# Kernel optimization log

Measured on AMD Instinct MI355X. Metric: run time of the kernel, lower is better.

Reference implementation:

```python
import jax, jax.numpy as jnp
import numpy as np

D = 1024        # n_embed
POS = 512       # n_pos_embed
H = 16          # heads
HS = D // H     # head size
DFF = 4 * D     # mlp hidden
EPS = 1e-5


def layernorm(x, g, b, eps=EPS):
    mu = jnp.mean(x, axis=-1, keepdims=True)
    var = jnp.var(x, axis=-1, keepdims=True)
    return (x - mu) * jax.lax.rsqrt(var + eps) * g + b


def setup_inputs() -> dict:
    key = jax.random.key(0)
    ks = jax.random.split(key, 12)
    std = 0.02
    inp = {
        "grid": jax.random.normal(ks[0], (8, 24, 24, D), dtype=jnp.float32),
        "query_pos": jax.random.normal(ks[1], (8, 1024, POS), dtype=jnp.float32),
        "Wq": jax.random.normal(ks[2], (POS, D), dtype=jnp.float32) * std,
        "Wk": jax.random.normal(ks[3], (D, D), dtype=jnp.float32) * std,
        "Wv": jax.random.normal(ks[4], (D, D), dtype=jnp.float32) * std,
        "Wo": jax.random.normal(ks[5], (D, D), dtype=jnp.float32) * std,
        "ln_grid_g": jnp.ones((D,), jnp.float32),
        "ln_grid_b": jnp.zeros((D,), jnp.float32),
        "ln_q_g": jnp.ones((POS,), jnp.float32),
        "ln_q_b": jnp.zeros((POS,), jnp.float32),
        "ln_mlp_g": jnp.ones((D,), jnp.float32),
        "ln_mlp_b": jnp.zeros((D,), jnp.float32),
        "W1": jax.random.normal(ks[6], (D, DFF), dtype=jnp.float32) * std,
        "b1": jnp.zeros((DFF,), jnp.float32),
        "W2": jax.random.normal(ks[7], (DFF, D), dtype=jnp.float32) * std,
        "b2": jnp.zeros((D,), jnp.float32),
    }
    return inp


def reference(grid, query_pos, Wq, Wk, Wv, Wo, ln_grid_g, ln_grid_b,
              ln_q_g, ln_q_b, ln_mlp_g, ln_mlp_b, W1, b1, W2, b2):
    B, N, M, d = grid.shape
    T = N * M
    grid_flat = grid.reshape(B, T, d)
    grid_norm = layernorm(grid_flat, ln_grid_g, ln_grid_b)
    K = jnp.einsum('btd,de->bte', grid_norm, Wk)
    V = jnp.einsum('btd,de->bte', grid_norm, Wv)
    query_norm = layernorm(query_pos, ln_q_g, ln_q_b)
    Q = jnp.einsum('blp,pe->ble', query_norm, Wq)
    L = Q.shape[1]
    # split heads: (B, H, L, HS)
    Qh = Q.reshape(B, L, H, HS).transpose(0, 2, 1, 3)
    Kh = K.reshape(B, T, H, HS).transpose(0, 2, 1, 3)
    Vh = V.reshape(B, T, H, HS).transpose(0, 2, 1, 3)
    scale = 1.0 / np.sqrt(HS).astype(np.float32)
    scores = jnp.einsum('bhld,bhmd->bhlm', Qh, Kh) * scale
    probs = jax.nn.softmax(scores, axis=-1)
    attn = jnp.einsum('bhlm,bhmd->bhld', probs, Vh)
    attn = attn.transpose(0, 2, 1, 3).reshape(B, L, d)
    attn = jnp.einsum('bld,de->ble', attn, Wo)
    x = Q + attn  # Q_proj residual
    x_norm = layernorm(x, ln_mlp_g, ln_mlp_b)
    mlp = jax.nn.gelu(x_norm @ W1 + b1) @ W2 + b2
    return x + mlp
```

## Files before the change

### kernel.cpp

```cpp
#include <hip/hip_runtime.h>

typedef __bf16 bf16x8 __attribute__((ext_vector_type(8)));
typedef float  f32x4  __attribute__((ext_vector_type(4)));
typedef short  s16x8  __attribute__((ext_vector_type(8)));

__device__ __forceinline__ unsigned short f2b(float f) {
  unsigned int u = __float_as_uint(f);
  u += 0x7fffu + ((u >> 16) & 1u);
  return (unsigned short)(u >> 16);
}
__device__ __forceinline__ float b2f(unsigned short h) {
  return __uint_as_float(((unsigned int)h) << 16);
}

__device__ __forceinline__ void gload_lds16(const unsigned short* g, unsigned short* l) {
  __builtin_amdgcn_global_load_lds((const __attribute__((address_space(1))) void*)g,
                                   (__attribute__((address_space(3))) void*)l, 16, 0, 0);
}

__device__ __forceinline__ void bar() {
  __builtin_amdgcn_sched_barrier(0);
  asm volatile("" ::: "memory");
  __builtin_amdgcn_s_barrier();
  asm volatile("" ::: "memory");
  __builtin_amdgcn_sched_barrier(0);
}

#define WAIT_LGKM0 do { asm volatile("s_waitcnt lgkmcnt(0)" ::: "memory"); \
                        __builtin_amdgcn_sched_barrier(0); } while (0)

__global__ __launch_bounds__(256) void transpose_w(const float* __restrict__ in,
                                                   unsigned short* __restrict__ out,
                                                   int R, int C) {
  __shared__ float t[32][33];
  int c0 = blockIdx.x * 32, r0 = blockIdx.y * 32;
  int tx = threadIdx.x & 31, ty = threadIdx.x >> 5;
  for (int i = ty; i < 32; i += 8)
    t[i][tx] = in[(size_t)(r0 + i) * C + (c0 + tx)];
  __syncthreads();
  for (int i = ty; i < 32; i += 8)
    out[(size_t)(c0 + i) * R + (r0 + tx)] = f2b(t[tx][i]);
}

__global__ __launch_bounds__(256) void transpose_v(const unsigned short* __restrict__ V,
                                                   unsigned short* __restrict__ Vt,
                                                   int vstride) {
  __shared__ unsigned short tile[64][72];
  const int t0 = blockIdx.x * 64;
  const int d0 = blockIdx.y * 64;
  const int b  = blockIdx.z;
  const int tid = threadIdx.x;
  const int r = tid >> 3, c8 = tid & 7;
#pragma unroll
  for (int p = 0; p < 2; ++p) {
    int row = p * 32 + r;
    s16x8 v = *(const s16x8*)(V + ((size_t)(b * 576 + t0 + row) * vstride + d0 + c8 * 8));
    *(s16x8*)&tile[row][c8 * 8] = v;
  }
  __syncthreads();
#pragma unroll
  for (int p = 0; p < 2; ++p) {
    int drow = p * 32 + r;
    unsigned short tmp[8];
#pragma unroll
    for (int j = 0; j < 8; ++j) tmp[j] = tile[c8 * 8 + j][drow];
    *(s16x8*)(Vt + ((size_t)(b * 1024 + d0 + drow) * 576 + t0 + c8 * 8)) = *(const s16x8*)tmp;
  }
}

__global__ __launch_bounds__(256) void ln_kernel(const float* __restrict__ in,
                                                 const float* __restrict__ g,
                                                 const float* __restrict__ b,
                                                 unsigned short* __restrict__ out,
                                                 int cols) {
  int row = blockIdx.x;
  const float* x = in + (size_t)row * cols;
  float s = 0.f, s2 = 0.f;
  for (int c = threadIdx.x * 4; c < cols; c += 1024) {
    float4 v = *(const float4*)(x + c);
    s  += v.x + v.y + v.z + v.w;
    s2 += v.x * v.x + v.y * v.y + v.z * v.z + v.w * v.w;
  }
#pragma unroll
  for (int o = 32; o > 0; o >>= 1) { s += __shfl_down(s, o); s2 += __shfl_down(s2, o); }
  __shared__ float rs[4], rs2[4];
  int w = threadIdx.x >> 6;
  if ((threadIdx.x & 63) == 0) { rs[w] = s; rs2[w] = s2; }
  __syncthreads();
  s  = rs[0] + rs[1] + rs[2] + rs[3];
  s2 = rs2[0] + rs2[1] + rs2[2] + rs2[3];
  float inv  = 1.f / (float)cols;
  float mean = s * inv;
  float var  = s2 * inv - mean * mean;
  float rstd = rsqrtf(var + 1e-5f);
  unsigned short* outp = out + (size_t)row * cols;
  for (int c = threadIdx.x * 4; c < cols; c += 1024) {
    float4 v = *(const float4*)(x + c);
    ushort4 ov;
    ov.x = f2b((v.x - mean) * rstd * g[c + 0] + b[c + 0]);
    ov.y = f2b((v.y - mean) * rstd * g[c + 1] + b[c + 1]);
    ov.z = f2b((v.z - mean) * rstd * g[c + 2] + b[c + 2]);
    ov.w = f2b((v.w - mean) * rstd * g[c + 3] + b[c + 3]);
    *(ushort4*)(outp + c) = ov;
  }
}

template <int BM, int BIAS, int GELU, int RES, int OUTBF>
__global__ __launch_bounds__(512) void gemm256(const unsigned short* __restrict__ A,
                                               const unsigned short* __restrict__ Bt,
                                               float* __restrict__ Cf,
                                               unsigned short* __restrict__ Cb,
                                               const float* __restrict__ bias,
                                               const float* __restrict__ resf,
                                               const unsigned short* __restrict__ resb,
                                               int M, int N, int K) {
  constexpr int MF = BM / 32;
  constexpr int MH = MF / 2;
  constexpr int LA = BM / 128;
  __shared__ unsigned short L[2][(BM + 256) * 64];
  const int tid = threadIdx.x;
  const int w = tid >> 6, l = tid & 63;
  const int rl = l & 15, kb = l >> 4;
  const int wm = w >> 2, wn = w & 3;
  const int m0 = blockIdx.x * BM, n0 = blockIdx.y * 256;
  const int NT = K >> 6;
  const int colsw = ((l & 7) ^ (l >> 3)) * 8;
  const int lrow = l >> 3;

  auto stage = [&](int t, int half) {
    if (t >= NT) return;
    unsigned short* base = L[t & 1];
    if (half < 2) {
      const unsigned short* g = Bt + (size_t)(n0 + half * 128) * K + t * 64;
#pragma unroll
      for (int j = 0; j < 2; ++j) {
        int row = w * 16 + j * 8;
        gload_lds16(g + (size_t)(row + lrow) * K + colsw,
                    base + BM * 64 + half * 8192 + row * 64);
      }
    } else {
      const int h = half - 2;
      const unsigned short* g = A + (size_t)(m0 + h * (BM / 2)) * K + t * 64;
#pragma unroll
      for (int j = 0; j < LA; ++j) {
        int row = w * (8 * LA) + j * 8;
        gload_lds16(g + (size_t)(row + lrow) * K + colsw,
                    base + h * (BM / 2) * 64 + row * 64);
      }
    }
  };

  f32x4 acc[MF][4];
  f32x4 zz = {0.f, 0.f, 0.f, 0.f};
#pragma unroll
  for (int i = 0; i < MF; ++i)
#pragma unroll
    for (int j = 0; j < 4; ++j) acc[i][j] = zz;

  stage(0, 0); stage(0, 1); stage(0, 2); stage(0, 3);
  stage(1, 0); stage(1, 1); stage(1, 2);

  const int aoff = wm * (BM / 2) * 64;
  const int boff = BM * 64 + (wn >> 1) * 8192 + (wn & 1) * 64 * 64;

  for (int t = 0; t < NT; ++t) {
    const unsigned short* Lb = L[t & 1];
    if (t + 1 < NT) {
      if constexpr (LA == 2) asm volatile("s_waitcnt vmcnt(6)" ::: "memory");
      else                   asm volatile("s_waitcnt vmcnt(5)" ::: "memory");
    } else {
      asm volatile("s_waitcnt vmcnt(0)" ::: "memory");
    }
    __builtin_amdgcn_sched_barrier(0);
    bar();

    bf16x8 af[MH][2], bf[4][2];
#pragma unroll
    for (int mf = 0; mf < MH; ++mf)
#pragma unroll
      for (int kf = 0; kf < 2; ++kf)
        af[mf][kf] = *(const bf16x8*)(Lb + aoff + (mf * 16 + rl) * 64 +
                                      (((kf * 4 + kb) ^ (rl & 7)) * 8));
#pragma unroll
    for (int nf = 0; nf < 4; ++nf)
#pragma unroll
      for (int kf = 0; kf < 2; ++kf)
        bf[nf][kf] = *(const bf16x8*)(Lb + boff + (nf * 16 + rl) * 64 +
                                      (((kf * 4 + kb) ^ (rl & 7)) * 8));
    stage(t + 1, 3);
    WAIT_LGKM0;
    __builtin_amdgcn_s_setprio(1);
#pragma unroll
    for (int mf = 0; mf < MH; ++mf)
#pragma unroll
      for (int nf = 0; nf < 2; ++nf)
#pragma unroll
        for (int kf = 0; kf < 2; ++kf)
          acc[mf][nf] = __builtin_amdgcn_mfma_f32_16x16x32_bf16(af[mf][kf], bf[nf][kf], acc[mf][nf], 0, 0, 0);
    __builtin_amdgcn_s_setprio(0);
    bar();

    stage(t + 2, 0);
    __builtin_amdgcn_s_setprio(1);
#pragma unroll
    for (int mf = 0; mf < MH; ++mf)
#pragma unroll
      for (int nf = 2; nf < 4; ++nf)
#pragma unroll
        for (int kf = 0; kf < 2; ++kf)
          acc[mf][nf] = __builtin_amdgcn_mfma_f32_16x16x32_bf16(af[mf][kf], bf[nf][kf], acc[mf][nf], 0, 0, 0);
    __builtin_amdgcn_s_setprio(0);
    bar();

#pragma unroll
    for (int mf = 0; mf < MH; ++mf)
#pragma unroll
      for (int kf = 0; kf < 2; ++kf)
        af[mf][kf] = *(const bf16x8*)(Lb + aoff + ((MH + mf) * 16 + rl) * 64 +
                                      (((kf * 4 + kb) ^ (rl & 7)) * 8));
    stage(t + 2, 1);
    WAIT_LGKM0;
    __builtin_amdgcn_s_setprio(1);
#pragma unroll
    for (int mf = 0; mf < MH; ++mf)
#pragma unroll
      for (int nf = 0; nf < 2; ++nf)
#pragma unroll
        for (int kf = 0; kf < 2; ++kf)
          acc[MH + mf][nf] = __builtin_amdgcn_mfma_f32_16x16x32_bf16(af[mf][kf], bf[nf][kf], acc[MH + mf][nf], 0, 0, 0);
    __builtin_amdgcn_s_setprio(0);
    bar();

    stage(t + 2, 2);
    __builtin_amdgcn_s_setprio(1);
#pragma unroll
    for (int mf = 0; mf < MH; ++mf)
#pragma unroll
      for (int nf = 2; nf < 4; ++nf)
#pragma unroll
        for (int kf = 0; kf < 2; ++kf)
          acc[MH + mf][nf] = __builtin_amdgcn_mfma_f32_16x16x32_bf16(af[mf][kf], bf[nf][kf], acc[MH + mf][nf], 0, 0, 0);
    __builtin_amdgcn_s_setprio(0);
  }

  bar();

  float bias_v[4];
  if (BIAS) {
#pragma unroll
    for (int nf = 0; nf < 4; ++nf) bias_v[nf] = bias[n0 + wn * 64 + nf * 16 + rl];
  }
  unsigned short* patch  = ((unsigned short*)L) + w * (16 * 72);
  float*          patchf = ((float*)L) + w * (16 * 72);

#pragma unroll
  for (int mf = 0; mf < MF; ++mf) {
#pragma unroll
    for (int nf = 0; nf < 4; ++nf) {
#pragma unroll
      for (int r = 0; r < 4; ++r) {
        float v = acc[mf][nf][r];
        if (BIAS) v += bias_v[nf];
        if (GELU) {
          float t2 = 1.5957691f * (v + 0.044715f * v * v * v);
          float e = __expf(fminf(t2, 60.f));
          v = v * e / (e + 1.f);
        }
        int prow = kb * 4 + r, pcol = nf * 16 + rl;
        if (OUTBF) patch[prow * 72 + pcol] = f2b(v);
        else       patchf[prow * 72 + pcol] = v;
      }
    }
    WAIT_LGKM0;
    if (OUTBF) {
#pragma unroll
      for (int half = 0; half < 2; ++half) {
        int prow = half * 8 + (l >> 3);
        int pcol = (l & 7) * 8;
        s16x8 vv = *(const s16x8*)(patch + prow * 72 + pcol);
        int grow = m0 + wm * (BM / 2) + mf * 16 + prow;
        int gcol = n0 + wn * 64 + pcol;
        *(s16x8*)(Cb + (size_t)grow * N + gcol) = vv;
      }
    } else {
#pragma unroll
      for (int p = 0; p < 4; ++p) {
        int prow = p * 4 + (l >> 4);
        int pcol = (l & 15) * 4;
        float4 vv = *(const float4*)(patchf + prow * 72 + pcol);
        int grow = m0 + wm * (BM / 2) + mf * 16 + prow;
        int gcol = n0 + wn * 64 + pcol;
        if (RES == 1) {
          float4 rv = *(const float4*)(resf + (size_t)grow * N + gcol);
          vv.x += rv.x; vv.y += rv.y; vv.z += rv.z; vv.w += rv.w;
        }
        if (RES == 2) {
          ushort4 rv = *(const ushort4*)(resb + (size_t)grow * N + gcol);
          vv.x += b2f(rv.x); vv.y += b2f(rv.y); vv.z += b2f(rv.z); vv.w += b2f(rv.w);
        }
        *(float4*)(Cf + (size_t)grow * N + gcol) = vv;
      }
    }
    WAIT_LGKM0;
  }
}

__global__ __launch_bounds__(256) void attn_mfma(const unsigned short* __restrict__ Qb,
                                                 const unsigned short* __restrict__ Kb,
                                                 const unsigned short* __restrict__ Vtb,
                                                 unsigned short* __restrict__ Ob,
                                                 int kstride) {
  __shared__ unsigned short Qs[64 * 64];
  __shared__ unsigned short Ks[2][64 * 64];
  __shared__ unsigned short Vs[2][64 * 64];
  __shared__ unsigned short Ps[64 * 64];

  const int t = threadIdx.x, w = t >> 6, l = t & 63;
  const int b = blockIdx.z, h = blockIdx.y, q0 = blockIdx.x * 64;
  const int rl = l & 15, kb = l >> 4;

  auto stage64 = [&](unsigned short* lds, const unsigned short* g, int gstride) {
#pragma unroll
    for (int p = 0; p < 2; ++p) {
      int row = p * 32 + w * 8 + (l >> 3);
      const unsigned short* src = g + (size_t)row * gstride + (((l & 7) ^ (row & 7)) * 8);
      gload_lds16(src, lds + p * 2048 + w * 512);
    }
  };

  const unsigned short* Qg = Qb + ((size_t)(b * 1024 + q0) * 1024 + h * 64);
  auto Kg = [&](int kt) { return Kb + ((size_t)(b * 576 + kt * 64) * kstride + h * 64); };
  auto Vg = [&](int kt) { return Vtb + ((size_t)(b * 1024 + h * 64) * 576 + kt * 64); };

  stage64(Qs, Qg, 1024);
  stage64(Ks[0], Kg(0), kstride);
  stage64(Vs[0], Vg(0), 576);
  __syncthreads();

  bf16x8 qf[2];
  {
    int row = w * 16 + rl;
#pragma unroll
    for (int kf = 0; kf < 2; ++kf)
      qf[kf] = *(const bf16x8*)(Qs + row * 64 + (((kf * 4 + kb) ^ (row & 7)) * 8));
  }

  float m_run[4], l_run[4];
  f32x4 accO[4];
#pragma unroll
  for (int r = 0; r < 4; ++r) { m_run[r] = -1e30f; l_run[r] = 0.f; }
  f32x4 zz = {0.f, 0.f, 0.f, 0.f};
#pragma unroll
  for (int nf = 0; nf < 4; ++nf) accO[nf] = zz;

  for (int kt = 0; kt < 9; ++kt) {
    const int buf = kt & 1;
    if (kt + 1 < 9) {
      stage64(Ks[buf ^ 1], Kg(kt + 1), kstride);
      stage64(Vs[buf ^ 1], Vg(kt + 1), 576);
    }

    f32x4 accS[4];
#pragma unroll
    for (int nf = 0; nf < 4; ++nf) accS[nf] = zz;
#pragma unroll
    for (int nf = 0; nf < 4; ++nf) {
      int row = nf * 16 + rl;
#pragma unroll
      for (int kf = 0; kf < 2; ++kf) {
        bf16x8 kfrag = *(const bf16x8*)(Ks[buf] + row * 64 + (((kf * 4 + kb) ^ (row & 7)) * 8));
        accS[nf] = __builtin_amdgcn_mfma_f32_16x16x32_bf16(qf[kf], kfrag, accS[nf], 0, 0, 0);
      }
    }

    float sv[4][4];
#pragma unroll
    for (int nf = 0; nf < 4; ++nf)
#pragma unroll
      for (int r = 0; r < 4; ++r) sv[nf][r] = accS[nf][r] * 0.125f;

    float al[4];
#pragma unroll
    for (int r = 0; r < 4; ++r) {
      float mr = fmaxf(fmaxf(sv[0][r], sv[1][r]), fmaxf(sv[2][r], sv[3][r]));
#pragma unroll
      for (int xm = 1; xm < 16; xm <<= 1) mr = fmaxf(mr, __shfl_xor(mr, xm));
      float mn = fmaxf(m_run[r], mr);
      al[r] = __expf(m_run[r] - mn);
      m_run[r] = mn;
      float rs = 0.f;
#pragma unroll
      for (int nf = 0; nf < 4; ++nf) {
        sv[nf][r] = __expf(sv[nf][r] - mn);
        rs += sv[nf][r];
      }
#pragma unroll
      for (int xm = 1; xm < 16; xm <<= 1) rs += __shfl_xor(rs, xm);
      l_run[r] = l_run[r] * al[r] + rs;
    }

#pragma unroll
    for (int nf = 0; nf < 4; ++nf)
#pragma unroll
      for (int r = 0; r < 4; ++r) {
        int q = w * 16 + kb * 4 + r;
        int col = nf * 16 + rl;
        Ps[q * 64 + (col ^ ((q & 7) << 3))] = f2b(sv[nf][r]);
      }

#pragma unroll
    for (int nf = 0; nf < 4; ++nf)
#pragma unroll
      for (int r = 0; r < 4; ++r) accO[nf][r] *= al[r];

    asm volatile("s_waitcnt lgkmcnt(0)" ::: "memory");
    __builtin_amdgcn_sched_barrier(0);

    bf16x8 pf[2];
    {
      int row = w * 16 + rl;
#pragma unroll
      for (int kf = 0; kf < 2; ++kf)
        pf[kf] = *(const bf16x8*)(Ps + row * 64 + (((kf * 4 + kb) ^ (row & 7)) * 8));
    }
#pragma unroll
    for (int nf = 0; nf < 4; ++nf) {
      int row = nf * 16 + rl;
#pragma unroll
      for (int kf = 0; kf < 2; ++kf) {
        bf16x8 vfrag = *(const bf16x8*)(Vs[buf] + row * 64 + (((kf * 4 + kb) ^ (row & 7)) * 8));
        accO[nf] = __builtin_amdgcn_mfma_f32_16x16x32_bf16(pf[kf], vfrag, accO[nf], 0, 0, 0);
      }
    }

    __syncthreads();
  }

#pragma unroll
  for (int nf = 0; nf < 4; ++nf) {
#pragma unroll
    for (int r = 0; r < 4; ++r) {
      float o = accO[nf][r] / l_run[r];
      size_t qg = (size_t)(b * 1024 + q0 + w * 16 + kb * 4 + r);
      Ob[qg * 1024 + h * 64 + nf * 16 + rl] = f2b(o);
    }
  }
}

extern "C" void kernel_launch(void* const* d_in, const int* in_sizes, int n_in,
                              void* d_out, int out_size, void* d_ws, size_t ws_size,
                              hipStream_t stream) {
  const float* grid_in = (const float*)d_in[0];
  const float* qpos    = (const float*)d_in[1];
  const float* Wq      = (const float*)d_in[2];
  const float* Wk      = (const float*)d_in[3];
  const float* Wv      = (const float*)d_in[4];
  const float* Wo      = (const float*)d_in[5];
  const float* g_grid  = (const float*)d_in[6];
  const float* b_grid  = (const float*)d_in[7];
  const float* g_q     = (const float*)d_in[8];
  const float* b_q     = (const float*)d_in[9];
  const float* g_mlp   = (const float*)d_in[10];
  const float* b_mlp   = (const float*)d_in[11];
  const float* W1      = (const float*)d_in[12];
  const float* b1      = (const float*)d_in[13];
  const float* W2      = (const float*)d_in[14];
  const float* b2      = (const float*)d_in[15];

  char* ws = (char*)d_ws;
  size_t off = 0;
  auto alloc = [&](size_t bytes) -> void* {
    void* p = ws + off;
    off = (off + bytes + 255) & ~(size_t)255;
    return p;
  };

  unsigned short* Wqt  = (unsigned short*)alloc((size_t)1024 * 512 * 2);
  unsigned short* Wkvt = (unsigned short*)alloc((size_t)2048 * 1024 * 2);
  unsigned short* Wot  = (unsigned short*)alloc((size_t)1024 * 1024 * 2);
  unsigned short* W1t  = (unsigned short*)alloc((size_t)4096 * 1024 * 2);
  unsigned short* W2t  = (unsigned short*)alloc((size_t)1024 * 4096 * 2);
  unsigned short* gn   = (unsigned short*)alloc((size_t)4608 * 1024 * 2);
  unsigned short* qn   = (unsigned short*)alloc((size_t)8192 * 512 * 2);
  unsigned short* KVb  = (unsigned short*)alloc((size_t)4608 * 2048 * 2);
  unsigned short* Qbf  = (unsigned short*)alloc((size_t)8192 * 1024 * 2);
  unsigned short* atb  = (unsigned short*)alloc((size_t)8192 * 1024 * 2);
  float*          xf   = (float*)alloc((size_t)8192 * 1024 * 4);
  unsigned short* xnb  = (unsigned short*)alloc((size_t)8192 * 1024 * 2);
  unsigned short* hb   = (unsigned short*)alloc((size_t)8192 * 4096 * 2);
  unsigned short* Vtb  = hb;
  (void)ws_size; (void)in_sizes; (void)n_in; (void)out_size;

  transpose_w<<<dim3(32, 16), 256, 0, stream>>>(Wq, Wqt, 512, 1024);
  transpose_w<<<dim3(32, 32), 256, 0, stream>>>(Wk, Wkvt, 1024, 1024);
  transpose_w<<<dim3(32, 32), 256, 0, stream>>>(Wv, Wkvt + (size_t)1024 * 1024, 1024, 1024);
  transpose_w<<<dim3(32, 32), 256, 0, stream>>>(Wo, Wot, 1024, 1024);
  transpose_w<<<dim3(128, 32), 256, 0, stream>>>(W1, W1t, 1024, 4096);
  transpose_w<<<dim3(32, 128), 256, 0, stream>>>(W2, W2t, 4096, 1024);

  ln_kernel<<<4608, 256, 0, stream>>>(grid_in, g_grid, b_grid, gn, 1024);
  ln_kernel<<<8192, 256, 0, stream>>>(qpos, g_q, b_q, qn, 512);

  gemm256<128, 0, 0, 0, 1><<<dim3(36, 8), 512, 0, stream>>>(gn, Wkvt, nullptr, KVb, nullptr, nullptr, nullptr, 4608, 2048, 1024);
  gemm256<128, 0, 0, 0, 1><<<dim3(64, 4), 512, 0, stream>>>(qn, Wqt, nullptr, Qbf, nullptr, nullptr, nullptr, 8192, 1024, 512);

  transpose_v<<<dim3(9, 16, 8), 256, 0, stream>>>(KVb + 1024, Vtb, 2048);

  attn_mfma<<<dim3(16, 16, 8), 256, 0, stream>>>(Qbf, KVb, Vtb, atb, 2048);

  gemm256<128, 0, 0, 2, 0><<<dim3(64, 4), 512, 0, stream>>>(atb, Wot, xf, nullptr, nullptr, nullptr, Qbf, 8192, 1024, 1024);

  ln_kernel<<<8192, 256, 0, stream>>>(xf, g_mlp, b_mlp, xnb, 1024);
  gemm256<256, 1, 1, 0, 1><<<dim3(32, 16), 512, 0, stream>>>(xnb, W1t, nullptr, hb, b1, nullptr, nullptr, 8192, 4096, 1024);
  gemm256<128, 1, 0, 1, 0><<<dim3(64, 4), 512, 0, stream>>>(hb, W2t, (float*)d_out, nullptr, b2, xf, nullptr, 8192, 1024, 4096);
}
```

Baseline: 368.6 us.

## Fuse K/V/Q projections into one launch, compute V transposed, transpose attention tiles

Merges the K, V and Q projection GEMMs into a single kernel that dispatches by block index. V is produced already transposed by swapping operands (Wv times grid_norm), so the separate transpose_v kernel is removed. Attention now computes S^T and O^T, which gives per-lane softmax rows with only two cross-lane shuffles and per-warp P tiles, and writes output as 4-wide vectors. This removes a kernel launch and an extra pass over V, and improves load balance, at the cost of a larger heterogeneous kernel and changed indexing.

```diff
diff --git a/kernel.cpp b/kernel.cpp
--- a/kernel.cpp
+++ b/kernel.cpp
@@ -40,32 +40,6 @@
   __syncthreads();
   for (int i = ty; i < 32; i += 8)
     out[(size_t)(c0 + i) * R + (r0 + tx)] = f2b(t[tx][i]);
-}
-
-__global__ __launch_bounds__(256) void transpose_v(const unsigned short* __restrict__ V,
-                                                   unsigned short* __restrict__ Vt,
-                                                   int vstride) {
-  __shared__ unsigned short tile[64][72];
-  const int t0 = blockIdx.x * 64;
-  const int d0 = blockIdx.y * 64;
-  const int b  = blockIdx.z;
-  const int tid = threadIdx.x;
-  const int r = tid >> 3, c8 = tid & 7;
-#pragma unroll
-  for (int p = 0; p < 2; ++p) {
-    int row = p * 32 + r;
-    s16x8 v = *(const s16x8*)(V + ((size_t)(b * 576 + t0 + row) * vstride + d0 + c8 * 8));
-    *(s16x8*)&tile[row][c8 * 8] = v;
-  }
-  __syncthreads();
-#pragma unroll
-  for (int p = 0; p < 2; ++p) {
-    int drow = p * 32 + r;
-    unsigned short tmp[8];
-#pragma unroll
-    for (int j = 0; j < 8; ++j) tmp[j] = tile[c8 * 8 + j][drow];
-    *(s16x8*)(Vt + ((size_t)(b * 1024 + d0 + drow) * 576 + t0 + c8 * 8)) = *(const s16x8*)tmp;
-  }
 }
 
 __global__ __launch_bounds__(256) void ln_kernel(const float* __restrict__ in,
@@ -106,30 +80,30 @@
 }
 
 template <int BM, int BIAS, int GELU, int RES, int OUTBF>
-__global__ __launch_bounds__(512) void gemm256(const unsigned short* __restrict__ A,
-                                               const unsigned short* __restrict__ Bt,
-                                               float* __restrict__ Cf,
-                                               unsigned short* __restrict__ Cb,
-                                               const float* __restrict__ bias,
-                                               const float* __restrict__ resf,
-                                               const unsigned short* __restrict__ resb,
-                                               int M, int N, int K) {
+__device__ __forceinline__ void gemm_body(const unsigned short* __restrict__ A,
+                                          const unsigned short* __restrict__ Bt,
+                                          float* __restrict__ Cf,
+                                          unsigned short* __restrict__ Cb,
+                                          const float* __restrict__ bias,
+                                          const float* __restrict__ resf,
+                                          const unsigned short* __restrict__ resb,
+                                          int N, int K, int m0, int n0,
+                                          unsigned short* L) {
   constexpr int MF = BM / 32;
   constexpr int MH = MF / 2;
   constexpr int LA = BM / 128;
-  __shared__ unsigned short L[2][(BM + 256) * 64];
+  constexpr int LSTEP = (BM + 256) * 64;
   const int tid = threadIdx.x;
   const int w = tid >> 6, l = tid & 63;
   const int rl = l & 15, kb = l >> 4;
   const int wm = w >> 2, wn = w & 3;
-  const int m0 = blockIdx.x * BM, n0 = blockIdx.y * 256;
   const int NT = K >> 6;
   const int colsw = ((l & 7) ^ (l >> 3)) * 8;
   const int lrow = l >> 3;
 
   auto stage = [&](int t, int half) {
     if (t >= NT) return;
-    unsigned short* base = L[t & 1];
+    unsigned short* base = L + (t & 1) * LSTEP;
     if (half < 2) {
       const unsigned short* g = Bt + (size_t)(n0 + half * 128) * K + t * 64;
 #pragma unroll
@@ -164,7 +138,7 @@
   const int boff = BM * 64 + (wn >> 1) * 8192 + (wn & 1) * 64 * 64;
 
   for (int t = 0; t < NT; ++t) {
-    const unsigned short* Lb = L[t & 1];
+    const unsigned short* Lb = L + (t & 1) * LSTEP;
     if (t + 1 < NT) {
       if constexpr (LA == 2) asm volatile("s_waitcnt vmcnt(6)" ::: "memory");
       else                   asm volatile("s_waitcnt vmcnt(5)" ::: "memory");
@@ -250,7 +224,7 @@
 #pragma unroll
     for (int nf = 0; nf < 4; ++nf) bias_v[nf] = bias[n0 + wn * 64 + nf * 16 + rl];
   }
-  unsigned short* patch  = ((unsigned short*)L) + w * (16 * 72);
+  unsigned short* patch  = L + w * (16 * 72);
   float*          patchf = ((float*)L) + w * (16 * 72);
 
 #pragma unroll
@@ -305,15 +279,52 @@
   }
 }
 
+template <int BM, int BIAS, int GELU, int RES, int OUTBF>
+__global__ __launch_bounds__(512) void gemm256(const unsigned short* __restrict__ A,
+                                               const unsigned short* __restrict__ Bt,
+                                               float* __restrict__ Cf,
+                                               unsigned short* __restrict__ Cb,
+                                               const float* __restrict__ bias,
+                                               const float* __restrict__ resf,
+                                               const unsigned short* __restrict__ resb,
+                                               int N, int K) {
+  __shared__ unsigned short L[2 * (BM + 256) * 64];
+  gemm_body<BM, BIAS, GELU, RES, OUTBF>(A, Bt, Cf, Cb, bias, resf, resb, N, K,
+                                        blockIdx.x * BM, blockIdx.y * 256, L);
+}
+
+__global__ __launch_bounds__(512) void kvq_gemm(const unsigned short* __restrict__ gn,
+                                                const unsigned short* __restrict__ Wkt,
+                                                unsigned short* __restrict__ Kb,
+                                                const unsigned short* __restrict__ Wvt,
+                                                unsigned short* __restrict__ Vt2,
+                                                const unsigned short* __restrict__ qn,
+                                                const unsigned short* __restrict__ Wqt,
+                                                unsigned short* __restrict__ Qbf) {
+  __shared__ unsigned short L[2 * (128 + 256) * 64];
+  const int x = blockIdx.x;
+  if (x < 144) {
+    gemm_body<128, 0, 0, 0, 1>(gn, Wkt, nullptr, Kb, nullptr, nullptr, nullptr,
+                               1024, 1024, (x % 36) * 128, (x / 36) * 256, L);
+  } else if (x < 288) {
+    const int x2 = x - 144;
+    gemm_body<128, 0, 0, 0, 1>(Wvt, gn, nullptr, Vt2, nullptr, nullptr, nullptr,
+                               4608, 1024, (x2 % 8) * 128, (x2 / 8) * 256, L);
+  } else {
+    const int x3 = x - 288;
+    gemm_body<128, 0, 0, 0, 1>(qn, Wqt, nullptr, Qbf, nullptr, nullptr, nullptr,
+                               1024, 512, (x3 % 64) * 128, (x3 / 64) * 256, L);
+  }
+}
+
 __global__ __launch_bounds__(256) void attn_mfma(const unsigned short* __restrict__ Qb,
                                                  const unsigned short* __restrict__ Kb,
                                                  const unsigned short* __restrict__ Vtb,
-                                                 unsigned short* __restrict__ Ob,
-                                                 int kstride) {
+                                                 unsigned short* __restrict__ Ob) {
   __shared__ unsigned short Qs[64 * 64];
   __shared__ unsigned short Ks[2][64 * 64];
   __shared__ unsigned short Vs[2][64 * 64];
-  __shared__ unsigned short Ps[64 * 64];
+  __shared__ unsigned short PsT[4][16 * 64];
 
   const int t = threadIdx.x, w = t >> 6, l = t & 63;
   const int b = blockIdx.z, h = blockIdx.y, q0 = blockIdx.x * 64;
@@ -329,12 +340,12 @@
   };
 
   const unsigned short* Qg = Qb + ((size_t)(b * 1024 + q0) * 1024 + h * 64);
-  auto Kg = [&](int kt) { return Kb + ((size_t)(b * 576 + kt * 64) * kstride + h * 64); };
-  auto Vg = [&](int kt) { return Vtb + ((size_t)(b * 1024 + h * 64) * 576 + kt * 64); };
+  auto Kg = [&](int kt) { return Kb + ((size_t)(b * 576 + kt * 64) * 1024 + h * 64); };
+  auto Vg = [&](int kt) { return Vtb + ((size_t)(h * 64) * 4608 + b * 576 + kt * 64); };
 
   stage64(Qs, Qg, 1024);
-  stage64(Ks[0], Kg(0), kstride);
-  stage64(Vs[0], Vg(0), 576);
+  stage64(Ks[0], Kg(0), 1024);
+  stage64(Vs[0], Vg(0), 4608);
   __syncthreads();
 
   bf16x8 qf[2];
@@ -345,19 +356,19 @@
       qf[kf] = *(const bf16x8*)(Qs + row * 64 + (((kf * 4 + kb) ^ (row & 7)) * 8));
   }
 
-  float m_run[4], l_run[4];
-  f32x4 accO[4];
-#pragma unroll
-  for (int r = 0; r < 4; ++r) { m_run[r] = -1e30f; l_run[r] = 0.f; }
+  float m_run = -1e30f, l_run = 0.f;
+  f32x4 accOT[4];
   f32x4 zz = {0.f, 0.f, 0.f, 0.f};
 #pragma unroll
-  for (int nf = 0; nf < 4; ++nf) accO[nf] = zz;
+  for (int df = 0; df < 4; ++df) accOT[df] = zz;
+
+  unsigned short* pw = &PsT[w][0];
 
   for (int kt = 0; kt < 9; ++kt) {
     const int buf = kt & 1;
     if (kt + 1 < 9) {
-      stage64(Ks[buf ^ 1], Kg(kt + 1), kstride);
-      stage64(Vs[buf ^ 1], Vg(kt + 1), 576);
+      stage64(Ks[buf ^ 1], Kg(kt + 1), 1024);
+      stage64(Vs[buf ^ 1], Vg(kt + 1), 4608);
     }
 
     f32x4 accS[4];
@@ -369,7 +380,7 @@
 #pragma unroll
       for (int kf = 0; kf < 2; ++kf) {
         bf16x8 kfrag = *(const bf16x8*)(Ks[buf] + row * 64 + (((kf * 4 + kb) ^ (row & 7)) * 8));
-        accS[nf] = __builtin_amdgcn_mfma_f32_16x16x32_bf16(qf[kf], kfrag, accS[nf], 0, 0, 0);
+        accS[nf] = __builtin_amdgcn_mfma_f32_16x16x32_bf16(kfrag, qf[kf], accS[nf], 0, 0, 0);
       }
     }
 
@@ -379,71 +390,70 @@
 #pragma unroll
       for (int r = 0; r < 4; ++r) sv[nf][r] = accS[nf][r] * 0.125f;
 
-    float al[4];
-#pragma unroll
-    for (int r = 0; r < 4; ++r) {
-      float mr = fmaxf(fmaxf(sv[0][r], sv[1][r]), fmaxf(sv[2][r], sv[3][r]));
-#pragma unroll
-      for (int xm = 1; xm < 16; xm <<= 1) mr = fmaxf(mr, __shfl_xor(mr, xm));
-      float mn = fmaxf(m_run[r], mr);
-      al[r] = __expf(m_run[r] - mn);
-      m_run[r] = mn;
-      float rs = 0.f;
-#pragma unroll
-      for (int nf = 0; nf < 4; ++nf) {
+    float rm = -1e30f;
+#pragma unroll
+    for (int nf = 0; nf < 4; ++nf)
+#pragma unroll
+      for (int r = 0; r < 4; ++r) rm = fmaxf(rm, sv[nf][r]);
+    rm = fmaxf(rm, __shfl_xor(rm, 16));
+    rm = fmaxf(rm, __shfl_xor(rm, 32));
+    float mn = fmaxf(m_run, rm);
+    float al = __expf(m_run - mn);
+    m_run = mn;
+    float rs = 0.f;
+#pragma unroll
+    for (int nf = 0; nf < 4; ++nf)
+#pragma unroll
+      for (int r = 0; r < 4; ++r) {
         sv[nf][r] = __expf(sv[nf][r] - mn);
         rs += sv[nf][r];
       }
-#pragma unroll
-      for (int xm = 1; xm < 16; xm <<= 1) rs += __shfl_xor(rs, xm);
-      l_run[r] = l_run[r] * al[r] + rs;
-    }
+    rs += __shfl_xor(rs, 16);
+    rs += __shfl_xor(rs, 32);
+    l_run = l_run * al + rs;
 
 #pragma unroll
     for (int nf = 0; nf < 4; ++nf)
 #pragma unroll
       for (int r = 0; r < 4; ++r) {
-        int q = w * 16 + kb * 4 + r;
-        int col = nf * 16 + rl;
-        Ps[q * 64 + (col ^ ((q & 7) << 3))] = f2b(sv[nf][r]);
-      }
-
-#pragma unroll
-    for (int nf = 0; nf < 4; ++nf)
-#pragma unroll
-      for (int r = 0; r < 4; ++r) accO[nf][r] *= al[r];
-
-    asm volatile("s_waitcnt lgkmcnt(0)" ::: "memory");
-    __builtin_amdgcn_sched_barrier(0);
+        int k = nf * 16 + kb * 4 + r;
+        pw[rl * 64 + (((k >> 3) ^ (rl & 7)) * 8) + (k & 7)] = f2b(sv[nf][r]);
+      }
+
+#pragma unroll
+    for (int df = 0; df < 4; ++df)
+#pragma unroll
+      for (int r = 0; r < 4; ++r) accOT[df][r] *= al;
+
+    WAIT_LGKM0;
 
     bf16x8 pf[2];
-    {
-      int row = w * 16 + rl;
-#pragma unroll
-      for (int kf = 0; kf < 2; ++kf)
-        pf[kf] = *(const bf16x8*)(Ps + row * 64 + (((kf * 4 + kb) ^ (row & 7)) * 8));
-    }
-#pragma unroll
-    for (int nf = 0; nf < 4; ++nf) {
-      int row = nf * 16 + rl;
-#pragma unroll
-      for (int kf = 0; kf < 2; ++kf) {
-        bf16x8 vfrag = *(const bf16x8*)(Vs[buf] + row * 64 + (((kf * 4 + kb) ^ (row & 7)) * 8));
-        accO[nf] = __builtin_amdgcn_mfma_f32_16x16x32_bf16(pf[kf], vfrag, accO[nf], 0, 0, 0);
+#pragma unroll
+    for (int ks = 0; ks < 2; ++ks)
+      pf[ks] = *(const bf16x8*)(pw + rl * 64 + (((ks * 4 + kb) ^ (rl & 7)) * 8));
+#pragma unroll
+    for (int df = 0; df < 4; ++df) {
+      int row = df * 16 + rl;
+#pragma unroll
+      for (int ks = 0; ks < 2; ++ks) {
+        bf16x8 vfrag = *(const bf16x8*)(Vs[buf] + row * 64 + (((ks * 4 + kb) ^ (row & 7)) * 8));
+        accOT[df] = __builtin_amdgcn_mfma_f32_16x16x32_bf16(vfrag, pf[ks], accOT[df], 0, 0, 0);
       }
     }
 
     __syncthreads();
   }
 
-#pragma unroll
-  for (int nf = 0; nf < 4; ++nf) {
-#pragma unroll
-    for (int r = 0; r < 4; ++r) {
-      float o = accO[nf][r] / l_run[r];
-      size_t qg = (size_t)(b * 1024 + q0 + w * 16 + kb * 4 + r);
-      Ob[qg * 1024 + h * 64 + nf * 16 + rl] = f2b(o);
-    }
+  float linv = 1.f / l_run;
+#pragma unroll
+  for (int df = 0; df < 4; ++df) {
+    ushort4 ov;
+    ov.x = f2b(accOT[df][0] * linv);
+    ov.y = f2b(accOT[df][1] * linv);
+    ov.z = f2b(accOT[df][2] * linv);
+    ov.w = f2b(accOT[df][3] * linv);
+    size_t qg = (size_t)(b * 1024 + q0 + w * 16 + rl);
+    *(ushort4*)(Ob + qg * 1024 + h * 64 + df * 16 + kb * 4) = ov;
   }
 }
 
@@ -475,25 +485,26 @@
     return p;
   };
 
-  unsigned short* Wqt  = (unsigned short*)alloc((size_t)1024 * 512 * 2);
-  unsigned short* Wkvt = (unsigned short*)alloc((size_t)2048 * 1024 * 2);
-  unsigned short* Wot  = (unsigned short*)alloc((size_t)1024 * 1024 * 2);
-  unsigned short* W1t  = (unsigned short*)alloc((size_t)4096 * 1024 * 2);
-  unsigned short* W2t  = (unsigned short*)alloc((size_t)1024 * 4096 * 2);
-  unsigned short* gn   = (unsigned short*)alloc((size_t)4608 * 1024 * 2);
-  unsigned short* qn   = (unsigned short*)alloc((size_t)8192 * 512 * 2);
-  unsigned short* KVb  = (unsigned short*)alloc((size_t)4608 * 2048 * 2);
-  unsigned short* Qbf  = (unsigned short*)alloc((size_t)8192 * 1024 * 2);
-  unsigned short* atb  = (unsigned short*)alloc((size_t)8192 * 1024 * 2);
-  float*          xf   = (float*)alloc((size_t)8192 * 1024 * 4);
-  unsigned short* xnb  = (unsigned short*)alloc((size_t)8192 * 1024 * 2);
-  unsigned short* hb   = (unsigned short*)alloc((size_t)8192 * 4096 * 2);
-  unsigned short* Vtb  = hb;
+  unsigned short* Wqt = (unsigned short*)alloc((size_t)1024 * 512 * 2);
+  unsigned short* Wkt = (unsigned short*)alloc((size_t)1024 * 1024 * 2);
+  unsigned short* Wvt = (unsigned short*)alloc((size_t)1024 * 1024 * 2);
+  unsigned short* Wot = (unsigned short*)alloc((size_t)1024 * 1024 * 2);
+  unsigned short* W1t = (unsigned short*)alloc((size_t)4096 * 1024 * 2);
+  unsigned short* W2t = (unsigned short*)alloc((size_t)1024 * 4096 * 2);
+  unsigned short* gn  = (unsigned short*)alloc((size_t)4608 * 1024 * 2);
+  unsigned short* qn  = (unsigned short*)alloc((size_t)8192 * 512 * 2);
+  unsigned short* Kb  = (unsigned short*)alloc((size_t)4608 * 1024 * 2);
+  unsigned short* Qbf = (unsigned short*)alloc((size_t)8192 * 1024 * 2);
+  unsigned short* atb = (unsigned short*)alloc((size_t)8192 * 1024 * 2);
+  float*          xf  = (float*)alloc((size_t)8192 * 1024 * 4);
+  unsigned short* xnb = (unsigned short*)alloc((size_t)8192 * 1024 * 2);
+  unsigned short* hb  = (unsigned short*)alloc((size_t)8192 * 4096 * 2);
+  unsigned short* Vt2 = hb;
   (void)ws_size; (void)in_sizes; (void)n_in; (void)out_size;
 
   transpose_w<<<dim3(32, 16), 256, 0, stream>>>(Wq, Wqt, 512, 1024);
-  transpose_w<<<dim3(32, 32), 256, 0, stream>>>(Wk, Wkvt, 1024, 1024);
-  transpose_w<<<dim3(32, 32), 256, 0, stream>>>(Wv, Wkvt + (size_t)1024 * 1024, 1024, 1024);
+  transpose_w<<<dim3(32, 32), 256, 0, stream>>>(Wk, Wkt, 1024, 1024);
+  transpose_w<<<dim3(32, 32), 256, 0, stream>>>(Wv, Wvt, 1024, 1024);
   transpose_w<<<dim3(32, 32), 256, 0, stream>>>(Wo, Wot, 1024, 1024);
   transpose_w<<<dim3(128, 32), 256, 0, stream>>>(W1, W1t, 1024, 4096);
   transpose_w<<<dim3(32, 128), 256, 0, stream>>>(W2, W2t, 4096, 1024);
@@ -501,16 +512,13 @@
   ln_kernel<<<4608, 256, 0, stream>>>(grid_in, g_grid, b_grid, gn, 1024);
   ln_kernel<<<8192, 256, 0, stream>>>(qpos, g_q, b_q, qn, 512);
 
-  gemm256<128, 0, 0, 0, 1><<<dim3(36, 8), 512, 0, stream>>>(gn, Wkvt, nullptr, KVb, nullptr, nullptr, nullptr, 4608, 2048, 1024);
-  gemm256<128, 0, 0, 0, 1><<<dim3(64, 4), 512, 0, stream>>>(qn, Wqt, nullptr, Qbf, nullptr, nullptr, nullptr, 8192, 1024, 512);
-
-  transpose_v<<<dim3(9, 16, 8), 256, 0, stream>>>(KVb + 1024, Vtb, 2048);
-
-  attn_mfma<<<dim3(16, 16, 8), 256, 0, stream>>>(Qbf, KVb, Vtb, atb, 2048);
-
-  gemm256<128, 0, 0, 2, 0><<<dim3(64, 4), 512, 0, stream>>>(atb, Wot, xf, nullptr, nullptr, nullptr, Qbf, 8192, 1024, 1024);
+  kvq_gemm<<<544, 512, 0, stream>>>(gn, Wkt, Kb, Wvt, Vt2, qn, Wqt, Qbf);
+
+  attn_mfma<<<dim3(16, 16, 8), 256, 0, stream>>>(Qbf, Kb, Vt2, atb);
+
+  gemm256<128, 0, 0, 2, 0><<<dim3(64, 4), 512, 0, stream>>>(atb, Wot, xf, nullptr, nullptr, nullptr, Qbf, 1024, 1024);
 
   ln_kernel<<<8192, 256, 0, stream>>>(xf, g_mlp, b_mlp, xnb, 1024);
-  gemm256<256, 1, 1, 0, 1><<<dim3(32, 16), 512, 0, stream>>>(xnb, W1t, nullptr, hb, b1, nullptr, nullptr, 8192, 4096, 1024);
-  gemm256<128, 1, 0, 1, 0><<<dim3(64, 4), 512, 0, stream>>>(hb, W2t, (float*)d_out, nullptr, b2, xf, nullptr, 8192, 1024, 4096);
-}
+  gemm256<256, 1, 1, 0, 1><<<dim3(32, 16), 512, 0, stream>>>(xnb, W1t, nullptr, hb, b1, nullptr, nullptr, 4096, 1024);
+  gemm256<128, 1, 0, 1, 0><<<dim3(64, 4), 512, 0, stream>>>(hb, W2t, (float*)d_out, nullptr, b2, xf, nullptr, 1024, 4096);
+}
```

Measured after the change: 351.5 us. 1.05x faster.
